# Optimization experiments

Hardware: AMD Instinct MI355X
Metric: run time of the kernel (lower is better)

Reference implementation:

```python
import jax, jax.numpy as jnp
import numpy as np

B, S, DM = 2, 2048, 1024
H, D = 16, 64  # num_heads, head_dim
EPS = 1e-5


def setup_inputs() -> dict:
    key = jax.random.key(0)
    ks = jax.random.split(key, 5)
    sc = 1.0 / np.sqrt(DM)
    return {
        "x": jax.random.normal(ks[0], (B, S, DM), jnp.float32),
        "wq": jax.random.normal(ks[1], (DM, DM), jnp.float32) * sc,
        "bq": jnp.zeros((DM,), jnp.float32),
        "wk": jax.random.normal(ks[2], (DM, DM), jnp.float32) * sc,
        "bk": jnp.zeros((DM,), jnp.float32),
        "wv": jax.random.normal(ks[3], (DM, DM), jnp.float32) * sc,
        "bv": jnp.zeros((DM,), jnp.float32),
        "wo": jax.random.normal(ks[4], (DM, DM), jnp.float32) * sc,
        "bo": jnp.zeros((DM,), jnp.float32),
        "alpha": jnp.ones((1,), jnp.float32),
    }


def reference(x, wq, bq, wk, bk, wv, bv, wo, bo, alpha):
    b, s, _ = x.shape
    # QKV projections -> [B, S, H, D]
    q = (x @ wq + bq).reshape(b, s, H, D)
    k = (x @ wk + bk).reshape(b, s, H, D)
    v = (x @ wv + bv).reshape(b, s, H, D)
    # YAT scores: (Q.K)^2 / (||Q-K||^2 + eps)
    dot = jnp.einsum("bqhd,bkhd->bhqk", q, k)  # [B,H,S,S]
    qn = jnp.einsum("bqhd,bqhd->bhq", q, q)    # ||q||^2
    kn = jnp.einsum("bkhd,bkhd->bhk", k, k)    # ||k||^2
    dist2 = qn[..., :, None] + kn[..., None, :] - 2.0 * dot
    scores = (dot * dot) / (dist2 + EPS)
    # alpha scaling: (sqrt(D)/log(1+D))^alpha
    scale = (jnp.sqrt(jnp.float32(D)) / jnp.log1p(jnp.float32(D))) ** alpha[0]
    attn = jax.nn.softmax(scores * scale, axis=-1)
    out = jnp.einsum("bhqk,bkhd->bqhd", attn, v).reshape(b, s, H * D)
    return out @ wo + bo
```

## Files before the change

### kernel.cpp

```cpp
#include <hip/hip_runtime.h>
#include <hip/hip_bf16.h>
#include <math.h>

typedef __bf16 bf16;
typedef bf16 bf16x4 __attribute__((ext_vector_type(4)));
typedef bf16 bf16x8 __attribute__((ext_vector_type(8)));
typedef float floatx4 __attribute__((ext_vector_type(4)));
typedef float floatx16 __attribute__((ext_vector_type(16)));

#define MFMA16(a, b, c) __builtin_amdgcn_mfma_f32_16x16x32_bf16(a, b, c, 0, 0, 0)
#define MFMA32(a, b, c) __builtin_amdgcn_mfma_f32_32x32x16_bf16(a, b, c, 0, 0, 0)

__device__ __forceinline__ void split2(float v, bf16& h, bf16& l) {
    h = (bf16)v;
    l = (bf16)(v - (float)h);
}

__device__ __forceinline__ unsigned cvt_pk(float lo, float hi) {
    unsigned r;
    asm("v_cvt_pk_bf16_f32 %0, %1, %2" : "=v"(r) : "v"(lo), "v"(hi));
    return r;
}

__device__ __forceinline__ void pl32swap(unsigned& a, unsigned& b) {
    asm("v_permlane32_swap_b32 %0, %1" : "+v"(a), "+v"(b));
}

__device__ __forceinline__ void gload16(const bf16* g, bf16* l) {
    __builtin_amdgcn_global_load_lds(
        (const __attribute__((address_space(1))) void*)g,
        (__attribute__((address_space(3))) void*)l, 16, 0, 0);
}

__global__ void prep_kernel(const float* __restrict__ xf,
                            const float* __restrict__ wq, const float* __restrict__ wk,
                            const float* __restrict__ wv, const float* __restrict__ wo,
                            bf16* __restrict__ xh, bf16* __restrict__ xl,
                            bf16* __restrict__ wt_qkv_h, bf16* __restrict__ wt_qkv_l,
                            bf16* __restrict__ wt_o_h) {
    const int z = blockIdx.z;
    if (z == 4) {
        const int tid = threadIdx.y * 32 + threadIdx.x;
        const int bid = blockIdx.y * 32 + blockIdx.x;
        const size_t i = ((size_t)bid * 256 + tid) * 16;
#pragma unroll
        for (int half = 0; half < 2; half++) {
            float4 a = *(const float4*)(xf + i + half * 8);
            float4 b = *(const float4*)(xf + i + half * 8 + 4);
            bf16x8 oh, ol;
            float f[8] = {a.x, a.y, a.z, a.w, b.x, b.y, b.z, b.w};
#pragma unroll
            for (int j = 0; j < 8; j++) { bf16 h, l; split2(f[j], h, l); oh[j] = h; ol[j] = l; }
            *(bf16x8*)(xh + i + half * 8) = oh;
            *(bf16x8*)(xl + i + half * 8) = ol;
        }
        return;
    }
    const float* src = (z == 0) ? wq : (z == 1) ? wk : (z == 2) ? wv : wo;
    bf16* dsth = (z < 3) ? (wt_qkv_h + (size_t)z * 1024 * 1024) : wt_o_h;
    bf16* dstl = (z < 3) ? (wt_qkv_l + (size_t)z * 1024 * 1024) : nullptr;
    __shared__ float tile[32][33];
    const int x0 = blockIdx.x * 32, y0 = blockIdx.y * 32;
    const int tx = threadIdx.x, ty = threadIdx.y;
    for (int i = 0; i < 32; i += 8)
        tile[ty + i][tx] = src[(size_t)(y0 + ty + i) * 1024 + x0 + tx];
    __syncthreads();
    for (int i = 0; i < 32; i += 8) {
        bf16 h, l;
        split2(tile[tx][ty + i], h, l);
        dsth[(size_t)(x0 + ty + i) * 1024 + y0 + tx] = h;
        if (dstl) dstl[(size_t)(x0 + ty + i) * 1024 + y0 + tx] = l;
    }
}

__global__ __launch_bounds__(256, 2) void gemm_qk3(
    const bf16* __restrict__ Ah, const bf16* __restrict__ Al,
    const bf16* __restrict__ Bth, const bf16* __restrict__ Btl,
    const float* __restrict__ bq, const float* __restrict__ bk,
    bf16* __restrict__ Qh, bf16* __restrict__ Ql,
    bf16* __restrict__ Kh, bf16* __restrict__ Kl) {
    __shared__ bf16 Ash[128 * 32];
    __shared__ bf16 Asl[128 * 32];
    __shared__ bf16 Bsh[128 * 32];
    __shared__ bf16 Bsl[128 * 32];

    const int t = threadIdx.x;
    const int lane = t & 63, wave = t >> 6;
    const int quad = lane >> 4, l16 = lane & 15;
    const int m0 = blockIdx.x * 128, n0 = blockIdx.y * 128;
    const int wm = (wave >> 1) * 64, wn = (wave & 1) * 64;

    const int srow = wave * 16 + (lane >> 2);
    const int scol = (lane & 3) * 8;
    const bf16* gAh = Ah + (size_t)(m0 + srow) * 1024 + scol;
    const bf16* gAl = Al + (size_t)(m0 + srow) * 1024 + scol;
    const bf16* gBh = Bth + (size_t)(n0 + srow) * 1024 + scol;
    const bf16* gBl = Btl + (size_t)(n0 + srow) * 1024 + scol;
    bf16* lAh = &Ash[wave * 16 * 32];
    bf16* lAl = &Asl[wave * 16 * 32];
    bf16* lBh = &Bsh[wave * 16 * 32];
    bf16* lBl = &Bsl[wave * 16 * 32];

    floatx4 acc[4][4] = {};

    for (int k0 = 0; k0 < 1024; k0 += 32) {
        gload16(gAh + k0, lAh);
        gload16(gAh + 64 * 1024 + k0, lAh + 64 * 32);
        gload16(gBh + k0, lBh);
        gload16(gBh + 64 * 1024 + k0, lBh + 64 * 32);
        gload16(gAl + k0, lAl);
        gload16(gAl + 64 * 1024 + k0, lAl + 64 * 32);
        gload16(gBl + k0, lBl);
        gload16(gBl + 64 * 1024 + k0, lBl + 64 * 32);
        __syncthreads();
        bf16x8 afh[4], bfh[4], afl[4], bfl[4];
#pragma unroll
        for (int i = 0; i < 4; i++) {
            afh[i] = *(bf16x8*)&Ash[(wm + i * 16 + l16) * 32 + quad * 8];
            afl[i] = *(bf16x8*)&Asl[(wm + i * 16 + l16) * 32 + quad * 8];
        }
#pragma unroll
        for (int j = 0; j < 4; j++) {
            bfh[j] = *(bf16x8*)&Bsh[(wn + j * 16 + l16) * 32 + quad * 8];
            bfl[j] = *(bf16x8*)&Bsl[(wn + j * 16 + l16) * 32 + quad * 8];
        }
#pragma unroll
        for (int i = 0; i < 4; i++)
#pragma unroll
            for (int j = 0; j < 4; j++) {
                acc[i][j] = MFMA16(afh[i], bfh[j], acc[i][j]);
                acc[i][j] = MFMA16(afh[i], bfl[j], acc[i][j]);
                acc[i][j] = MFMA16(afl[i], bfh[j], acc[i][j]);
            }
        __syncthreads();
    }

    const int which = n0 >> 10;
    const float* bias = (which == 0) ? bq : bk;
    bf16* Dh = (which == 0) ? Qh : Kh;
    bf16* Dl = (which == 0) ? Ql : Kl;
#pragma unroll
    for (int i = 0; i < 4; i++)
#pragma unroll
        for (int j = 0; j < 4; j++) {
            const int col = n0 + wn + j * 16 + l16;
            const int o = col & 1023;
            const int h = o >> 6, d = o & 63;
            const float bvv = bias[o];
            const int gm0 = m0 + wm + i * 16 + quad * 4;
            const int b = gm0 >> 11;
#pragma unroll
            for (int r = 0; r < 4; r++) {
                const int gm = gm0 + r;
                const int s = gm & 2047;
                const size_t idx = (size_t)((b * 16 + h) * 2048 + s) * 64 + d;
                const float val = acc[i][j][r] + bvv;
                bf16 hi, lo;
                split2(val, hi, lo);
                Dh[idx] = hi;
                Dl[idx] = lo;
            }
        }
}

__global__ __launch_bounds__(256, 2) void gemm_v(
    const bf16* __restrict__ Ah, const bf16* __restrict__ Bth,
    const float* __restrict__ bv, bf16* __restrict__ VtG) {
    __shared__ bf16 As[128 * 32];
    __shared__ bf16 Bs[64 * 32];

    const int t = threadIdx.x;
    const int lane = t & 63, wave = t >> 6;
    const int quad = lane >> 4, l16 = lane & 15;
    const int m0 = blockIdx.x * 128, n0 = blockIdx.y * 64;
    const int wm = (wave >> 1) * 64, wn = (wave & 1) * 32;

    const int srow = wave * 16 + (lane >> 2);
    const int scol = (lane & 3) * 8;
    const bf16* gA0 = Ah + (size_t)(m0 + srow) * 1024 + scol;
    const bf16* gB0 = Bth + (size_t)(2048 + n0 + srow) * 1024 + scol;
    bf16* lA = &As[wave * 16 * 32];
    bf16* lB = &Bs[wave * 16 * 32];

    floatx4 acc[4][2] = {};

    for (int k0 = 0; k0 < 1024; k0 += 32) {
        gload16(gA0 + k0, lA);
        gload16(gA0 + 64 * 1024 + k0, lA + 64 * 32);
        gload16(gB0 + k0, lB);
        __syncthreads();
        bf16x8 af[4], bf_[2];
#pragma unroll
        for (int i = 0; i < 4; i++)
            af[i] = *(bf16x8*)&As[(wm + i * 16 + l16) * 32 + quad * 8];
#pragma unroll
        for (int j = 0; j < 2; j++)
            bf_[j] = *(bf16x8*)&Bs[(wn + j * 16 + l16) * 32 + quad * 8];
#pragma unroll
        for (int i = 0; i < 4; i++)
#pragma unroll
            for (int j = 0; j < 2; j++)
                acc[i][j] = MFMA16(af[i], bf_[j], acc[i][j]);
        __syncthreads();
    }

#pragma unroll
    for (int i = 0; i < 4; i++)
#pragma unroll
        for (int j = 0; j < 2; j++) {
            const int o = (n0 + wn + j * 16 + l16) & 1023;
            const int h = o >> 6, d = o & 63;
            const float bvv = bv[o];
            const int gm0 = m0 + wm + i * 16 + quad * 4;
            const int b = gm0 >> 11;
            bf16x4 pv;
#pragma unroll
            for (int r = 0; r < 4; r++) pv[r] = (bf16)(acc[i][j][r] + bvv);
            const int s0 = gm0 & 2047;
            *(bf16x4*)&VtG[((size_t)((b * 16 + h) * 64 + d)) * 2048 + s0] = pv;
        }
}

__global__ void kn_kernel(const bf16* __restrict__ Kh, const bf16* __restrict__ Kl,
                          float* __restrict__ knG) {
    const int i = blockIdx.x * 256 + threadIdx.x;
    const bf16* ph = Kh + (size_t)i * 64;
    const bf16* pl = Kl + (size_t)i * 64;
    float s = 0.f;
#pragma unroll
    for (int d0 = 0; d0 < 64; d0 += 8) {
        bf16x8 vh = *(const bf16x8*)(ph + d0);
        bf16x8 vl = *(const bf16x8*)(pl + d0);
#pragma unroll
        for (int j = 0; j < 8; j++) { float x = (float)vh[j] + (float)vl[j]; s += x * x; }
    }
    knG[i] = s;
}

__global__ __launch_bounds__(256, 2) void attn_kernel(
    const bf16* __restrict__ Qh, const bf16* __restrict__ Ql,
    const bf16* __restrict__ Kh, const bf16* __restrict__ Kl,
    const bf16* __restrict__ VtG, const float* __restrict__ knG,
    bf16* __restrict__ O, const float* __restrict__ alphap) {
    __shared__ bf16 Ksh[2][64 * 64];
    __shared__ bf16 Ksl[2][64 * 64];
    __shared__ bf16 Vs[2][64 * 64];
    __shared__ __align__(16) float knL[2][64];

    const int t = threadIdx.x, lane = t & 63, wave = t >> 6;
    const int l31 = lane & 31, h = lane >> 5;
    const int bh = blockIdx.x;
    const int qw = blockIdx.y * 128 + wave * 32;

    const float alpha = alphap[0];
    const float C = powf(8.0f / log1pf(64.0f), alpha) * 1.44269504f;

    const size_t qbase = ((size_t)bh * 2048 + qw + l31) * 64;
    bf16x8 bqh[4], bql[4];
#pragma unroll
    for (int cb = 0; cb < 4; cb++) {
        bqh[cb] = *(const bf16x8*)(Qh + qbase + cb * 16 + h * 8);
        bql[cb] = *(const bf16x8*)(Ql + qbase + cb * 16 + h * 8);
    }
    float qn = 0.f;
#pragma unroll
    for (int cb = 0; cb < 4; cb++)
#pragma unroll
        for (int j = 0; j < 8; j++) {
            float x = (float)bqh[cb][j] + (float)bql[cb][j];
            qn += x * x;
        }
    qn += __shfl_xor(qn, 32, 64);
    const float qne = qn + 1e-5f;

    floatx16 acco[2] = {};
    float l_run = 0.f;

    const int lrow = lane >> 3;
    const int lslot = (lane & 7) ^ lrow;
    const int r0 = wave * 16;
    const bf16* gK0 = Kh + ((size_t)bh * 2048 + r0 + lrow) * 64 + lslot * 8;
    const bf16* gK1 = Kl + ((size_t)bh * 2048 + r0 + lrow) * 64 + lslot * 8;
    const bf16* gV0 = VtG + ((size_t)bh * 64 + r0 + lrow) * 2048 + lslot * 8;
    const float* knB = knG + (size_t)bh * 2048;

    auto stage = [&](int ib, int kc) {
        gload16(gK0 + (size_t)kc * 64, &Ksh[ib][r0 * 64]);
        gload16(gK0 + (size_t)kc * 64 + 8 * 64, &Ksh[ib][(r0 + 8) * 64]);
        gload16(gK1 + (size_t)kc * 64, &Ksl[ib][r0 * 64]);
        gload16(gK1 + (size_t)kc * 64 + 8 * 64, &Ksl[ib][(r0 + 8) * 64]);
        gload16(gV0 + kc, &Vs[ib][r0 * 64]);
        gload16(gV0 + kc + 8 * 2048, &Vs[ib][(r0 + 8) * 64]);
    };

    const int fmask = (l31 & 7) * 8;
    int foff[2][4];
#pragma unroll
    for (int rb = 0; rb < 2; rb++)
#pragma unroll
        for (int cb = 0; cb < 4; cb++)
            foff[rb][cb] = (rb * 32 + l31) * 64 + ((cb * 16 + h * 8) ^ fmask);

    auto do_chunk = [&](int ib) {
        const bf16* KH = Ksh[ib];
        const bf16* KL = Ksl[ib];
        const bf16* VV = Vs[ib];
        const float* knC = knL[ib];

        floatx16 acc[2] = {};
        __builtin_amdgcn_s_setprio(1);
#pragma unroll
        for (int cb = 0; cb < 4; cb++)
#pragma unroll
            for (int kb = 0; kb < 2; kb++) {
                bf16x8 ah = *(const bf16x8*)&KH[foff[kb][cb]];
                bf16x8 al = *(const bf16x8*)&KL[foff[kb][cb]];
                acc[kb] = MFMA32(ah, bqh[cb], acc[kb]);
                acc[kb] = MFMA32(ah, bql[cb], acc[kb]);
                acc[kb] = MFMA32(al, bqh[cb], acc[kb]);
            }
        __builtin_amdgcn_s_setprio(0);

        unsigned pw[2][8];
        float rs = 0.f;
#pragma unroll
        for (int kb = 0; kb < 2; kb++) {
            float p[16];
#pragma unroll
            for (int g2 = 0; g2 < 4; g2++) {
                const floatx4 knv = *(const floatx4*)&knC[kb * 32 + g2 * 8 + h * 4];
#pragma unroll
                for (int j = 0; j < 4; j++) {
                    const int r = g2 * 4 + j;
                    const float d = acc[kb][r];
                    const float e = fmaf(-2.0f, d, qne + knv[j]);
                    const float s = fmaf(C * d * d, __builtin_amdgcn_rcpf(e), -110.0f);
                    const float pp = __builtin_amdgcn_exp2f(s);
                    rs += pp;
                    p[r] = pp;
                }
            }
#pragma unroll
            for (int g = 0; g < 2; g++) {
                unsigned a0 = cvt_pk(p[8 * g + 0], p[8 * g + 1]);
                unsigned a1 = cvt_pk(p[8 * g + 2], p[8 * g + 3]);
                unsigned b0 = cvt_pk(p[8 * g + 4], p[8 * g + 5]);
                unsigned b1 = cvt_pk(p[8 * g + 6], p[8 * g + 7]);
                pl32swap(a0, b0);
                pl32swap(a1, b1);
                pw[kb][g * 4 + 0] = a0;
                pw[kb][g * 4 + 1] = a1;
                pw[kb][g * 4 + 2] = b0;
                pw[kb][g * 4 + 3] = b1;
            }
        }
        l_run += rs;

        __builtin_amdgcn_s_setprio(1);
#pragma unroll
        for (int db = 0; db < 2; db++)
#pragma unroll
            for (int g4 = 0; g4 < 4; g4++) {
                bf16x8 vf = *(const bf16x8*)&VV[foff[db][g4]];
                union { unsigned u[4]; bf16x8 v; } pu;
                pu.u[0] = pw[g4 >> 1][(g4 & 1) * 4 + 0];
                pu.u[1] = pw[g4 >> 1][(g4 & 1) * 4 + 1];
                pu.u[2] = pw[g4 >> 1][(g4 & 1) * 4 + 2];
                pu.u[3] = pw[g4 >> 1][(g4 & 1) * 4 + 3];
                acco[db] = MFMA32(vf, pu.v, acco[db]);
            }
        __builtin_amdgcn_s_setprio(0);
    };

    stage(0, 0);
    if (t < 16) *(float4*)&knL[0][t * 4] = *(const float4*)(knB + t * 4);
    __syncthreads();

    for (int ic = 0; ic < 31; ic++) {
        const int cur = ic & 1, nxt = cur ^ 1;
        const int kc = (ic + 1) * 64;
        stage(nxt, kc);
        float4 nkn;
        if (t < 16) nkn = *(const float4*)(knB + kc + t * 4);

        do_chunk(cur);

        if (t < 16) *(float4*)&knL[nxt][t * 4] = nkn;
        __syncthreads();
    }
    do_chunk(1);

    const float l_tot = l_run + __shfl_xor(l_run, 32, 64);
    const float rl = 1.0f / l_tot;
    const int b = bh >> 4, hh = bh & 15;
    const int q = qw + l31;
    const size_t obase = (size_t)(b * 2048 + q) * 1024 + hh * 64;
#pragma unroll
    for (int db = 0; db < 2; db++)
#pragma unroll
        for (int g2 = 0; g2 < 4; g2++) {
            bf16x4 ov;
#pragma unroll
            for (int j = 0; j < 4; j++) ov[j] = (bf16)(acco[db][g2 * 4 + j] * rl);
            const int d = db * 32 + g2 * 8 + h * 4;
            *(bf16x4*)&O[obase + d] = ov;
        }
}

__global__ __launch_bounds__(256, 2) void gemm_out(
    const bf16* __restrict__ A, const bf16* __restrict__ Bt,
    const float* __restrict__ bias, float* __restrict__ outC) {
    __shared__ bf16 As[128 * 32];
    __shared__ bf16 Bs[64 * 32];

    const int t = threadIdx.x;
    const int lane = t & 63, wave = t >> 6;
    const int quad = lane >> 4, l16 = lane & 15;
    const int m0 = blockIdx.x * 128, n0 = blockIdx.y * 64;
    const int wm = (wave >> 1) * 64, wn = (wave & 1) * 32;

    const int srow = wave * 16 + (lane >> 2);
    const int scol = (lane & 3) * 8;
    const bf16* gA0 = A + (size_t)(m0 + srow) * 1024 + scol;
    const bf16* gB0 = Bt + (size_t)(n0 + srow) * 1024 + scol;
    bf16* lA = &As[wave * 16 * 32];
    bf16* lB = &Bs[wave * 16 * 32];

    floatx4 acc[4][2] = {};

    for (int k0 = 0; k0 < 1024; k0 += 32) {
        gload16(gA0 + k0, lA);
        gload16(gA0 + 64 * 1024 + k0, lA + 64 * 32);
        gload16(gB0 + k0, lB);
        __syncthreads();
        bf16x8 af[4], bf_[2];
#pragma unroll
        for (int i = 0; i < 4; i++)
            af[i] = *(bf16x8*)&As[(wm + i * 16 + l16) * 32 + quad * 8];
#pragma unroll
        for (int j = 0; j < 2; j++)
            bf_[j] = *(bf16x8*)&Bs[(wn + j * 16 + l16) * 32 + quad * 8];
#pragma unroll
        for (int i = 0; i < 4; i++)
#pragma unroll
            for (int j = 0; j < 2; j++)
                acc[i][j] = MFMA16(af[i], bf_[j], acc[i][j]);
        __syncthreads();
    }

#pragma unroll
    for (int i = 0; i < 4; i++)
#pragma unroll
        for (int j = 0; j < 2; j++) {
            const int col = n0 + wn + j * 16 + l16;
            const float bvv = bias[col];
#pragma unroll
            for (int r = 0; r < 4; r++) {
                const int gm = m0 + wm + i * 16 + quad * 4 + r;
                outC[(size_t)gm * 1024 + col] = acc[i][j][r] + bvv;
            }
        }
}

extern "C" void kernel_launch(void* const* d_in, const int* in_sizes, int n_in,
                              void* d_out, int out_size, void* d_ws, size_t ws_size,
                              hipStream_t stream) {
    const float* x  = (const float*)d_in[0];
    const float* wq = (const float*)d_in[1];
    const float* bq = (const float*)d_in[2];
    const float* wk = (const float*)d_in[3];
    const float* bk = (const float*)d_in[4];
    const float* wv = (const float*)d_in[5];
    const float* bv = (const float*)d_in[6];
    const float* wo = (const float*)d_in[7];
    const float* bo = (const float*)d_in[8];
    const float* alpha = (const float*)d_in[9];

    char* ws = (char*)d_ws;
    const size_t MB = 1024 * 1024;
    bf16* wqkv_h = (bf16*)(ws);
    bf16* wqkv_l = (bf16*)(ws + 6 * MB);
    bf16* wo_h   = (bf16*)(ws + 12 * MB);
    float* knG   = (float*)(ws + 14 * MB);
    bf16* x_h    = (bf16*)(ws + 16 * MB);
    bf16* x_l    = (bf16*)(ws + 24 * MB);
    bf16* Q_h    = (bf16*)(ws + 32 * MB);
    bf16* Q_l    = (bf16*)(ws + 40 * MB);
    bf16* K_h    = (bf16*)(ws + 48 * MB);
    bf16* K_l    = (bf16*)(ws + 56 * MB);
    bf16* Vt_g   = (bf16*)(ws + 64 * MB);
    bf16* Ob     = (bf16*)(ws);

    prep_kernel<<<dim3(32, 32, 5), dim3(32, 8), 0, stream>>>(
        x, wq, wk, wv, wo, x_h, x_l, wqkv_h, wqkv_l, wo_h);
    gemm_qk3<<<dim3(32, 16), 256, 0, stream>>>(
        x_h, x_l, wqkv_h, wqkv_l, bq, bk, Q_h, Q_l, K_h, K_l);
    gemm_v<<<dim3(32, 16), 256, 0, stream>>>(x_h, wqkv_h, bv, Vt_g);
    kn_kernel<<<dim3(256), 256, 0, stream>>>(K_h, K_l, knG);
    attn_kernel<<<dim3(32, 16), 256, 0, stream>>>(
        Q_h, Q_l, K_h, K_l, Vt_g, knG, Ob, alpha);
    gemm_out<<<dim3(32, 16), 256, 0, stream>>>(Ob, wo_h, bo, (float*)d_out);
}
```

Baseline: 283.7 us.

## Load K/V fragments directly from global memory instead of shared-memory staging

Removes the double-buffered LDS staging of K high/low, V and key norms, along with the per-chunk barriers and setprio hints. Each wave now reads its MFMA operand fragments straight from global memory, relying on the cache for reuse across the four waves. This drops the synchronization and LDS traffic but gives up explicit prefetch overlap and exposes global-load latency inside the loop.

```diff
diff --git a/kernel.cpp b/kernel.cpp
--- a/kernel.cpp
+++ b/kernel.cpp
@@ -242,11 +242,6 @@
     const bf16* __restrict__ Kh, const bf16* __restrict__ Kl,
     const bf16* __restrict__ VtG, const float* __restrict__ knG,
     bf16* __restrict__ O, const float* __restrict__ alphap) {
-    __shared__ bf16 Ksh[2][64 * 64];
-    __shared__ bf16 Ksl[2][64 * 64];
-    __shared__ bf16 Vs[2][64 * 64];
-    __shared__ __align__(16) float knL[2][64];
-
     const int t = threadIdx.x, lane = t & 63, wave = t >> 6;
     const int l31 = lane & 31, h = lane >> 5;
     const int bh = blockIdx.x;
@@ -276,50 +271,26 @@
     floatx16 acco[2] = {};
     float l_run = 0.f;
 
-    const int lrow = lane >> 3;
-    const int lslot = (lane & 7) ^ lrow;
-    const int r0 = wave * 16;
-    const bf16* gK0 = Kh + ((size_t)bh * 2048 + r0 + lrow) * 64 + lslot * 8;
-    const bf16* gK1 = Kl + ((size_t)bh * 2048 + r0 + lrow) * 64 + lslot * 8;
-    const bf16* gV0 = VtG + ((size_t)bh * 64 + r0 + lrow) * 2048 + lslot * 8;
-    const float* knB = knG + (size_t)bh * 2048;
-
-    auto stage = [&](int ib, int kc) {
-        gload16(gK0 + (size_t)kc * 64, &Ksh[ib][r0 * 64]);
-        gload16(gK0 + (size_t)kc * 64 + 8 * 64, &Ksh[ib][(r0 + 8) * 64]);
-        gload16(gK1 + (size_t)kc * 64, &Ksl[ib][r0 * 64]);
-        gload16(gK1 + (size_t)kc * 64 + 8 * 64, &Ksl[ib][(r0 + 8) * 64]);
-        gload16(gV0 + kc, &Vs[ib][r0 * 64]);
-        gload16(gV0 + kc + 8 * 2048, &Vs[ib][(r0 + 8) * 64]);
-    };
-
-    const int fmask = (l31 & 7) * 8;
-    int foff[2][4];
-#pragma unroll
-    for (int rb = 0; rb < 2; rb++)
+    const bf16* Kb = Kh + ((size_t)bh * 2048 + l31) * 64 + h * 8;
+    const bf16* Klb = Kl + ((size_t)bh * 2048 + l31) * 64 + h * 8;
+    const bf16* Vb = VtG + ((size_t)bh * 64 + l31) * 2048 + h * 8;
+    const float* knB = knG + (size_t)bh * 2048 + h * 4;
+
+    for (int ic = 0; ic < 32; ic++) {
+        const int kc = ic * 64;
+
+        floatx16 acc[2] = {};
 #pragma unroll
         for (int cb = 0; cb < 4; cb++)
-            foff[rb][cb] = (rb * 32 + l31) * 64 + ((cb * 16 + h * 8) ^ fmask);
-
-    auto do_chunk = [&](int ib) {
-        const bf16* KH = Ksh[ib];
-        const bf16* KL = Ksl[ib];
-        const bf16* VV = Vs[ib];
-        const float* knC = knL[ib];
-
-        floatx16 acc[2] = {};
-        __builtin_amdgcn_s_setprio(1);
-#pragma unroll
-        for (int cb = 0; cb < 4; cb++)
 #pragma unroll
             for (int kb = 0; kb < 2; kb++) {
-                bf16x8 ah = *(const bf16x8*)&KH[foff[kb][cb]];
-                bf16x8 al = *(const bf16x8*)&KL[foff[kb][cb]];
+                const size_t ko = (size_t)(kc + kb * 32) * 64 + cb * 16;
+                bf16x8 ah = *(const bf16x8*)(Kb + ko);
+                bf16x8 al = *(const bf16x8*)(Klb + ko);
                 acc[kb] = MFMA32(ah, bqh[cb], acc[kb]);
                 acc[kb] = MFMA32(ah, bql[cb], acc[kb]);
                 acc[kb] = MFMA32(al, bqh[cb], acc[kb]);
             }
-        __builtin_amdgcn_s_setprio(0);
 
         unsigned pw[2][8];
         float rs = 0.f;
@@ -328,7 +299,7 @@
             float p[16];
 #pragma unroll
             for (int g2 = 0; g2 < 4; g2++) {
-                const floatx4 knv = *(const floatx4*)&knC[kb * 32 + g2 * 8 + h * 4];
+                const floatx4 knv = *(const floatx4*)(knB + kc + kb * 32 + g2 * 8);
 #pragma unroll
                 for (int j = 0; j < 4; j++) {
                     const int r = g2 * 4 + j;
@@ -356,12 +327,11 @@
         }
         l_run += rs;
 
-        __builtin_amdgcn_s_setprio(1);
 #pragma unroll
         for (int db = 0; db < 2; db++)
 #pragma unroll
             for (int g4 = 0; g4 < 4; g4++) {
-                bf16x8 vf = *(const bf16x8*)&VV[foff[db][g4]];
+                bf16x8 vf = *(const bf16x8*)(Vb + (size_t)(db * 32) * 2048 + kc + g4 * 16);
                 union { unsigned u[4]; bf16x8 v; } pu;
                 pu.u[0] = pw[g4 >> 1][(g4 & 1) * 4 + 0];
                 pu.u[1] = pw[g4 >> 1][(g4 & 1) * 4 + 1];
@@ -369,26 +339,7 @@
                 pu.u[3] = pw[g4 >> 1][(g4 & 1) * 4 + 3];
                 acco[db] = MFMA32(vf, pu.v, acco[db]);
             }
-        __builtin_amdgcn_s_setprio(0);
-    };
-
-    stage(0, 0);
-    if (t < 16) *(float4*)&knL[0][t * 4] = *(const float4*)(knB + t * 4);
-    __syncthreads();
-
-    for (int ic = 0; ic < 31; ic++) {
-        const int cur = ic & 1, nxt = cur ^ 1;
-        const int kc = (ic + 1) * 64;
-        stage(nxt, kc);
-        float4 nkn;
-        if (t < 16) nkn = *(const float4*)(knB + kc + t * 4);
-
-        do_chunk(cur);
-
-        if (t < 16) *(float4*)&knL[nxt][t * 4] = nkn;
-        __syncthreads();
-    }
-    do_chunk(1);
+    }
 
     const float l_tot = l_run + __shfl_xor(l_run, 32, 64);
     const float rl = 1.0f / l_tot;
```

Result: slower. 391.2 us (+37.9%).
